# Kernel tuning notes

Hardware: AMD Instinct MI355X
Metric: run time of the kernel (lower is better)

Reference implementation:

```python
import jax, jax.numpy as jnp
import numpy as np

B, T, S, D, K = 512, 49, 200, 512, 128


def setup_inputs() -> dict:
    key = jax.random.key(0)
    ks = jax.random.split(key, 8)
    return {
        "ifeature": jax.random.normal(ks[0], (B, T, D), dtype=jnp.float32),
        "tfeature_h": jax.random.normal(ks[1], (B, S, D), dtype=jnp.float32),
        "w_Dense_Vi_0": jax.random.normal(ks[2], (D, K), dtype=jnp.float32) * 0.05,
        "w_Dense_Vt_0": jax.random.normal(ks[3], (D, K), dtype=jnp.float32) * 0.05,
        "w_Dense_Pi_0": jax.random.normal(ks[4], (2 * K, 1), dtype=jnp.float32) * 0.05,
        "b_Dense_Pi_0": jnp.zeros((T,), dtype=jnp.float32),
        "w_Dense_Vi_1": jax.random.normal(ks[5], (D, K), dtype=jnp.float32) * 0.05,
        "w_Dense_Vt_1": jax.random.normal(ks[6], (D, K), dtype=jnp.float32) * 0.05,
        "w_Dense_Pi_1": jax.random.normal(ks[7], (2 * K, 1), dtype=jnp.float32) * 0.05,
        "b_Dense_Pi_1": jnp.zeros((S,), dtype=jnp.float32),
    }


def reference(ifeature, tfeature_h, w_Dense_Vi_0, w_Dense_Vt_0, w_Dense_Pi_0,
              b_Dense_Pi_0, w_Dense_Vi_1, w_Dense_Vt_1, w_Dense_Pi_1, b_Dense_Pi_1):
    # tfeature: mean-pooled text, [B, D]
    tfeature = jnp.mean(tfeature_h, axis=1)

    # --- attention over image regions (title_len) ---
    w_Vi_0 = jnp.einsum('btd,dk->btk', ifeature, w_Dense_Vi_0)          # [B,T,K]
    w_Vt_0 = (tfeature @ w_Dense_Vt_0)[:, None, :]                      # [B,1,K] broadcast to T
    Hi = jnp.tanh(jnp.concatenate(
        [w_Vi_0, jnp.broadcast_to(w_Vt_0, w_Vi_0.shape)], axis=-1))     # [B,T,2K]
    Hi_w_b = jnp.einsum('btk,k->bt', Hi, w_Dense_Pi_0[:, 0]) + b_Dense_Pi_0
    Pi = jax.nn.softmax(Hi_w_b, axis=-1)                                # [B,T]
    Vi = jnp.einsum('bt,btd->bd', Pi, ifeature)                         # attended image feature

    # --- attention over text tokens (seq_len) ---
    w_Vi_1 = (Vi @ w_Dense_Vi_1)[:, None, :]                            # [B,1,K]
    w_Vt_1 = jnp.einsum('bsd,dk->bsk', tfeature_h, w_Dense_Vt_1)        # [B,S,K]
    Ht = jnp.tanh(jnp.concatenate(
        [jnp.broadcast_to(w_Vi_1, w_Vt_1.shape), w_Vt_1], axis=-1))     # [B,S,2K]
    Ht_b = jnp.einsum('bsk,k->bs', Ht, w_Dense_Pi_1[:, 0]) + b_Dense_Pi_1
    Pt = jax.nn.softmax(Ht_b, axis=-1)                                  # [B,S]

    # NOTE: original call() returns Pt_Vt (weighted tokens), not the pooled Vt.
    Pt_Vt = Pt[:, :, None] * tfeature_h                                 # [B,S,D]
    return Pt_Vt
```

## Files before the change

### kernel.cpp

```cpp
#include <hip/hip_runtime.h>
#include <math.h>

#define BB 512
#define SS 200
#define DD 512
#define KK 128
#define RR (BB * SS)

typedef __attribute__((ext_vector_type(8))) short bf16x8;
typedef __attribute__((ext_vector_type(4))) short bf16x4;
typedef __attribute__((ext_vector_type(4))) float f32x4;

__device__ inline unsigned short f2bf(float f) {
    union { float f; unsigned int u; } v; v.f = f;
    unsigned int r = v.u + 0x7FFFu + ((v.u >> 16) & 1u);
    return (unsigned short)(r >> 16);
}

__device__ inline float fast_tanh(float x) {
    x = fminf(10.f, fmaxf(-10.f, x));
    float t = exp2f(x * 2.885390081777927f);
    return (t - 1.f) * __builtin_amdgcn_rcpf(t + 1.f);
}

__global__ void wt_kernel(const float* __restrict__ W, unsigned short* __restrict__ Wt2) {
    int i = blockIdx.x * 256 + threadIdx.x;
    int j = i & 7;
    int l = (i >> 3) & 63;
    int n = (i >> 9) & 7;
    int t = i >> 12;
    int k = n * 16 + (l & 15);
    int d = t * 32 + (l >> 4) * 8 + j;
    Wt2[i] = f2bf(W[d * KK + k]);
}

__global__ __launch_bounds__(256, 4) void logits_kernel(
    const float* __restrict__ tfh,
    const unsigned short* __restrict__ Wt2,
    const float* __restrict__ wpk,
    const float* __restrict__ bias,
    float* __restrict__ logits)
{
    __shared__ unsigned short As[128][40];

    int tid = threadIdx.x;
    int w   = tid >> 6;
    int l   = tid & 63;
    int l15 = l & 15;
    int g   = l >> 4;
    int brow = blockIdx.x * 128;

    int r0 = tid >> 3;
    int c4 = tid & 7;
    const float* ap = tfh + (size_t)(brow + r0) * DD + c4 * 4;

    const unsigned short* bp = Wt2 + (size_t)l * 8;

    f32x4 acc[2][8];
    #pragma unroll
    for (int m = 0; m < 2; ++m)
        #pragma unroll
        for (int n = 0; n < 8; ++n) acc[m][n] = (f32x4){0.f, 0.f, 0.f, 0.f};

    for (int t = 0; t < 16; ++t) {
        int d0 = t * 32;
        #pragma unroll
        for (int jj = 0; jj < 4; ++jj) {
            float4 v = *(const float4*)(ap + d0 + (size_t)(32 * jj) * DD);
            bf16x4 p;
            p[0] = (short)f2bf(v.x); p[1] = (short)f2bf(v.y);
            p[2] = (short)f2bf(v.z); p[3] = (short)f2bf(v.w);
            *(bf16x4*)&As[r0 + 32 * jj][c4 * 4] = p;
        }
        __syncthreads();
        bf16x8 af0 = *(const bf16x8*)&As[w * 32 + l15][g * 8];
        bf16x8 af1 = *(const bf16x8*)&As[w * 32 + 16 + l15][g * 8];
        const unsigned short* bt = bp + (size_t)t * (8 * 64 * 8);
        #pragma unroll
        for (int nb = 0; nb < 4; ++nb) {
            bf16x8 b0 = *(const bf16x8*)(bt + (2 * nb) * 512);
            bf16x8 b1 = *(const bf16x8*)(bt + (2 * nb + 1) * 512);
            acc[0][2*nb]   = __builtin_amdgcn_mfma_f32_16x16x32_bf16(af0, b0, acc[0][2*nb],   0, 0, 0);
            acc[1][2*nb]   = __builtin_amdgcn_mfma_f32_16x16x32_bf16(af1, b0, acc[1][2*nb],   0, 0, 0);
            acc[0][2*nb+1] = __builtin_amdgcn_mfma_f32_16x16x32_bf16(af0, b1, acc[0][2*nb+1], 0, 0, 0);
            acc[1][2*nb+1] = __builtin_amdgcn_mfma_f32_16x16x32_bf16(af1, b1, acc[1][2*nb+1], 0, 0, 0);
        }
        __syncthreads();
    }

    float wv[8];
    #pragma unroll
    for (int n = 0; n < 8; ++n) wv[n] = wpk[n * 16 + l15];

    float rs[2][4];
    #pragma unroll
    for (int m = 0; m < 2; ++m)
        #pragma unroll
        for (int r = 0; r < 4; ++r) rs[m][r] = 0.f;
    #pragma unroll
    for (int m = 0; m < 2; ++m)
        #pragma unroll
        for (int n = 0; n < 8; ++n)
            #pragma unroll
            for (int r = 0; r < 4; ++r)
                rs[m][r] += fast_tanh(acc[m][n][r]) * wv[n];
    #pragma unroll
    for (int m = 0; m < 2; ++m)
        #pragma unroll
        for (int r = 0; r < 4; ++r) {
            float v = rs[m][r];
            v += __shfl_xor(v, 1, 64);
            v += __shfl_xor(v, 2, 64);
            v += __shfl_xor(v, 4, 64);
            v += __shfl_xor(v, 8, 64);
            rs[m][r] = v;
        }
    if (l15 == 0) {
        #pragma unroll
        for (int m = 0; m < 2; ++m)
            #pragma unroll
            for (int r = 0; r < 4; ++r) {
                int grow = brow + w * 32 + m * 16 + g * 4 + r;
                logits[grow] = rs[m][r] + bias[grow % SS];
            }
    }
}

__global__ __launch_bounds__(1024) void softmax_mul_kernel(
    const float* __restrict__ logits,
    const float* __restrict__ tfh,
    float* __restrict__ out)
{
    int b = blockIdx.x;
    int tid = threadIdx.x;
    __shared__ float Pt[SS];
    __shared__ float wpart[16];

    float v = (tid < SS) ? logits[(size_t)b * SS + tid] : -INFINITY;
    float m = v;
    #pragma unroll
    for (int off = 32; off > 0; off >>= 1) m = fmaxf(m, __shfl_xor(m, off, 64));
    if ((tid & 63) == 0) wpart[tid >> 6] = m;
    __syncthreads();
    m = -INFINITY;
    #pragma unroll
    for (int i = 0; i < 16; ++i) m = fmaxf(m, wpart[i]);
    float e = (tid < SS) ? expf(v - m) : 0.f;
    float ssum = e;
    #pragma unroll
    for (int off = 32; off > 0; off >>= 1) ssum += __shfl_xor(ssum, off, 64);
    __syncthreads();
    if ((tid & 63) == 0) wpart[tid >> 6] = ssum;
    __syncthreads();
    ssum = 0.f;
    #pragma unroll
    for (int i = 0; i < 16; ++i) ssum += wpart[i];
    if (tid < SS) Pt[tid] = e / ssum;
    __syncthreads();

    const f32x4* src = (const f32x4*)(tfh + (size_t)b * SS * DD);
    f32x4*       dst = (f32x4*)(out + (size_t)b * SS * DD);
    const int n4 = SS * DD / 4;
    for (int i = tid; i < n4; i += 1024) {
        float p = Pt[i >> 7];
        f32x4 x = src[i];
        x = x * p;
        __builtin_nontemporal_store(x, dst + i);
    }
}

extern "C" void kernel_launch(void* const* d_in, const int* in_sizes, int n_in,
                              void* d_out, int out_size, void* d_ws, size_t ws_size,
                              hipStream_t stream) {
    const float* tfh   = (const float*)d_in[1];
    const float* wVt1  = (const float*)d_in[7];
    const float* wp1   = (const float*)d_in[8];
    const float* bias1 = (const float*)d_in[9];
    float* out = (float*)d_out;

    unsigned short* Wt2 = (unsigned short*)d_ws;
    float* logits = (float*)((char*)d_ws + 16 * 8 * 64 * 8 * sizeof(unsigned short));

    wt_kernel<<<(16 * 8 * 64 * 8) / 256, 256, 0, stream>>>(wVt1, Wt2);
    logits_kernel<<<RR / 128, 256, 0, stream>>>(tfh, Wt2, wp1 + KK, bias1, logits);
    softmax_mul_kernel<<<BB, 1024, 0, stream>>>(logits, tfh, out);
}
```

Before: 116.5 us.

## Pre-convert activations to bf16 MFMA fragment layout and double-buffer weights in LDS

Adds a separate pass that converts tfeature_h to bf16 and stores it already in MFMA fragment order. A new logits kernel then loads A fragments straight from global memory with register prefetch, and stages the weights in double-buffered LDS so only one barrier is needed per k-step. This removes the in-kernel conversion and LDS round-trip for A. In exchange it costs an extra pass over the 210MB input that writes about 105MB of bf16, and it needs a large workspace, falling back to the old kernel when the workspace is too small.

```diff
diff --git a/kernel.cpp b/kernel.cpp
--- a/kernel.cpp
+++ b/kernel.cpp
@@ -15,6 +15,15 @@
     union { float f; unsigned int u; } v; v.f = f;
     unsigned int r = v.u + 0x7FFFu + ((v.u >> 16) & 1u);
     return (unsigned short)(r >> 16);
+}
+
+__device__ inline bf16x8 pack8(const float4& a, const float4& b) {
+    bf16x8 p;
+    p[0] = (short)f2bf(a.x); p[1] = (short)f2bf(a.y);
+    p[2] = (short)f2bf(a.z); p[3] = (short)f2bf(a.w);
+    p[4] = (short)f2bf(b.x); p[5] = (short)f2bf(b.y);
+    p[6] = (short)f2bf(b.z); p[7] = (short)f2bf(b.w);
+    return p;
 }
 
 __device__ inline float fast_tanh(float x) {
@@ -34,6 +43,120 @@
     Wt2[i] = f2bf(W[d * KK + k]);
 }
 
+__global__ __launch_bounds__(256) void conv_kernel(
+    const float* __restrict__ tfh, unsigned short* __restrict__ bfA)
+{
+    size_t i = (size_t)blockIdx.x * 256 + threadIdx.x;
+    int l   = (int)(i & 63);
+    int sub = (int)((i >> 6) & 7);
+    int t   = (int)((i >> 9) & 15);
+    size_t rt = i >> 13;
+    size_t row = rt * 128 + sub * 16 + (l & 15);
+    int d = t * 32 + (l >> 4) * 8;
+    const float* s = tfh + row * DD + d;
+    float4 v0 = *(const float4*)s;
+    float4 v1 = *(const float4*)(s + 4);
+    *(bf16x8*)(bfA + i * 8) = pack8(v0, v1);
+}
+
+__global__ __launch_bounds__(256, 4) void logits_frag2_kernel(
+    const unsigned short* __restrict__ bfA,
+    const unsigned short* __restrict__ Wt2,
+    const float* __restrict__ wpk,
+    const float* __restrict__ bias,
+    float* __restrict__ logits)
+{
+    __shared__ unsigned short Bs[2][4096];
+
+    int tid = threadIdx.x;
+    int w   = tid >> 6;
+    int l   = tid & 63;
+    int l15 = l & 15;
+    int g   = l >> 4;
+    int rt  = blockIdx.x;
+    int brow = rt * 128;
+
+    const unsigned short* ap = bfA + ((((size_t)rt * 16) * 8 + w * 2) * 64 + l) * 8;
+    const unsigned short* bsrc = Wt2 + tid * 16;
+
+    f32x4 acc[2][8];
+    #pragma unroll
+    for (int m = 0; m < 2; ++m)
+        #pragma unroll
+        for (int n = 0; n < 8; ++n) acc[m][n] = (f32x4){0.f, 0.f, 0.f, 0.f};
+
+    {
+        bf16x8 s0 = *(const bf16x8*)(bsrc);
+        bf16x8 s1 = *(const bf16x8*)(bsrc + 8);
+        *(bf16x8*)&Bs[0][tid * 16]     = s0;
+        *(bf16x8*)&Bs[0][tid * 16 + 8] = s1;
+    }
+    bf16x8 a0 = *(const bf16x8*)(ap);
+    bf16x8 a1 = *(const bf16x8*)(ap + 512);
+    __syncthreads();
+
+    for (int t = 0; t < 16; ++t) {
+        int buf = t & 1;
+        bf16x8 na0, na1, sb0, sb1;
+        if (t < 15) {
+            size_t off = (size_t)(t + 1) * 4096;
+            na0 = *(const bf16x8*)(ap + off);
+            na1 = *(const bf16x8*)(ap + off + 512);
+            sb0 = *(const bf16x8*)(bsrc + off);
+            sb1 = *(const bf16x8*)(bsrc + off + 8);
+        }
+        #pragma unroll
+        for (int n = 0; n < 8; ++n) {
+            bf16x8 bf = *(const bf16x8*)&Bs[buf][n * 512 + l * 8];
+            acc[0][n] = __builtin_amdgcn_mfma_f32_16x16x32_bf16(a0, bf, acc[0][n], 0, 0, 0);
+            acc[1][n] = __builtin_amdgcn_mfma_f32_16x16x32_bf16(a1, bf, acc[1][n], 0, 0, 0);
+        }
+        if (t < 15) {
+            *(bf16x8*)&Bs[buf ^ 1][tid * 16]     = sb0;
+            *(bf16x8*)&Bs[buf ^ 1][tid * 16 + 8] = sb1;
+        }
+        __syncthreads();
+        a0 = na0; a1 = na1;
+    }
+
+    float wv[8];
+    #pragma unroll
+    for (int n = 0; n < 8; ++n) wv[n] = wpk[n * 16 + l15];
+
+    float rs[2][4];
+    #pragma unroll
+    for (int m = 0; m < 2; ++m)
+        #pragma unroll
+        for (int r = 0; r < 4; ++r) rs[m][r] = 0.f;
+    #pragma unroll
+    for (int m = 0; m < 2; ++m)
+        #pragma unroll
+        for (int n = 0; n < 8; ++n)
+            #pragma unroll
+            for (int r = 0; r < 4; ++r)
+                rs[m][r] += fast_tanh(acc[m][n][r]) * wv[n];
+    #pragma unroll
+    for (int m = 0; m < 2; ++m)
+        #pragma unroll
+        for (int r = 0; r < 4; ++r) {
+            float v = rs[m][r];
+            v += __shfl_xor(v, 1, 64);
+            v += __shfl_xor(v, 2, 64);
+            v += __shfl_xor(v, 4, 64);
+            v += __shfl_xor(v, 8, 64);
+            rs[m][r] = v;
+        }
+    if (l15 == 0) {
+        #pragma unroll
+        for (int m = 0; m < 2; ++m)
+            #pragma unroll
+            for (int r = 0; r < 4; ++r) {
+                int grow = brow + w * 32 + m * 16 + g * 4 + r;
+                logits[grow] = rs[m][r] + bias[grow % SS];
+            }
+    }
+}
+
 __global__ __launch_bounds__(256, 4) void logits_kernel(
     const float* __restrict__ tfh,
     const unsigned short* __restrict__ Wt2,
@@ -42,18 +165,15 @@
     float* __restrict__ logits)
 {
     __shared__ unsigned short As[128][40];
-
     int tid = threadIdx.x;
     int w   = tid >> 6;
     int l   = tid & 63;
     int l15 = l & 15;
     int g   = l >> 4;
     int brow = blockIdx.x * 128;
-
     int r0 = tid >> 3;
     int c4 = tid & 7;
     const float* ap = tfh + (size_t)(brow + r0) * DD + c4 * 4;
-
     const unsigned short* bp = Wt2 + (size_t)l * 8;
 
     f32x4 acc[2][8];
@@ -91,7 +211,6 @@
     float wv[8];
     #pragma unroll
     for (int n = 0; n < 8; ++n) wv[n] = wpk[n * 16 + l15];
-
     float rs[2][4];
     #pragma unroll
     for (int m = 0; m < 2; ++m)
@@ -179,9 +298,16 @@
     float* out = (float*)d_out;
 
     unsigned short* Wt2 = (unsigned short*)d_ws;
-    float* logits = (float*)((char*)d_ws + 16 * 8 * 64 * 8 * sizeof(unsigned short));
+    float* logits = (float*)((char*)d_ws + (128 << 10));
+    unsigned short* bfA = (unsigned short*)((char*)d_ws + (1 << 20));
+    const size_t need = (size_t)(1 << 20) + (size_t)RR * DD * 2;
 
     wt_kernel<<<(16 * 8 * 64 * 8) / 256, 256, 0, stream>>>(wVt1, Wt2);
-    logits_kernel<<<RR / 128, 256, 0, stream>>>(tfh, Wt2, wp1 + KK, bias1, logits);
+    if (ws_size >= need) {
+        conv_kernel<<<(int)(((size_t)RR * DD / 8) / 256), 256, 0, stream>>>(tfh, bfA);
+        logits_frag2_kernel<<<RR / 128, 256, 0, stream>>>(bfA, Wt2, wp1 + KK, bias1, logits);
+    } else {
+        logits_kernel<<<RR / 128, 256, 0, stream>>>(tfh, Wt2, wp1 + KK, bias1, logits);
+    }
     softmax_mul_kernel<<<BB, 1024, 0, stream>>>(logits, tfh, out);
 }
```

After: 167.2 us. 1.43x slower.

## Stage weight tiles in shared memory and double the K-step per iteration

Applied to the files above, without the earlier changes.

The weight matrix is now stored as a plain transposed bf16 [K][D] array. Each block stages a 128x64 slice of it into LDS next to the activation tile, where before every wave read pre-swizzled fragments straight from global memory. The K-loop step grows from 32 to 64, which halves the number of barrier pairs, and the occupancy hint drops from 4 to 3 blocks to make room for the larger LDS footprint. The aim is fewer global/L2 weight reads and less synchronisation overhead, at the cost of more LDS use and possibly lower occupancy.

```diff
diff --git a/kernel.cpp b/kernel.cpp
--- a/kernel.cpp
+++ b/kernel.cpp
@@ -23,25 +23,21 @@
     return (t - 1.f) * __builtin_amdgcn_rcpf(t + 1.f);
 }
 
-__global__ void wt_kernel(const float* __restrict__ W, unsigned short* __restrict__ Wt2) {
+__global__ void wt_kernel(const float* __restrict__ W, unsigned short* __restrict__ Wt) {
     int i = blockIdx.x * 256 + threadIdx.x;
-    int j = i & 7;
-    int l = (i >> 3) & 63;
-    int n = (i >> 9) & 7;
-    int t = i >> 12;
-    int k = n * 16 + (l & 15);
-    int d = t * 32 + (l >> 4) * 8 + j;
-    Wt2[i] = f2bf(W[d * KK + k]);
+    int col = i >> 9, d = i & 511;
+    Wt[i] = f2bf(W[d * KK + col]);
 }
 
-__global__ __launch_bounds__(256, 4) void logits_kernel(
+__global__ __launch_bounds__(256, 3) void logits_kernel(
     const float* __restrict__ tfh,
-    const unsigned short* __restrict__ Wt2,
+    const unsigned short* __restrict__ Wt,
     const float* __restrict__ wpk,
     const float* __restrict__ bias,
     float* __restrict__ logits)
 {
-    __shared__ unsigned short As[128][40];
+    __shared__ unsigned short As[128][72];
+    __shared__ unsigned short Bs[128][72];
 
     int tid = threadIdx.x;
     int w   = tid >> 6;
@@ -50,11 +46,13 @@
     int g   = l >> 4;
     int brow = blockIdx.x * 128;
 
-    int r0 = tid >> 3;
-    int c4 = tid & 7;
-    const float* ap = tfh + (size_t)(brow + r0) * DD + c4 * 4;
+    int arow = tid >> 4;
+    int ac4  = tid & 15;
+    const float* ap = tfh + (size_t)(brow + arow) * DD + ac4 * 4;
 
-    const unsigned short* bp = Wt2 + (size_t)l * 8;
+    int bkrow = tid >> 3;
+    int bc8   = tid & 7;
+    const unsigned short* bp = Wt + (size_t)bkrow * DD + bc8 * 8;
 
     f32x4 acc[2][8];
     #pragma unroll
@@ -62,28 +60,32 @@
         #pragma unroll
         for (int n = 0; n < 8; ++n) acc[m][n] = (f32x4){0.f, 0.f, 0.f, 0.f};
 
-    for (int t = 0; t < 16; ++t) {
-        int d0 = t * 32;
+    for (int it = 0; it < 8; ++it) {
+        int d0 = it * 64;
         #pragma unroll
-        for (int jj = 0; jj < 4; ++jj) {
-            float4 v = *(const float4*)(ap + d0 + (size_t)(32 * jj) * DD);
+        for (int j = 0; j < 8; ++j) {
+            float4 v = *(const float4*)(ap + d0 + (size_t)(16 * j) * DD);
             bf16x4 p;
             p[0] = (short)f2bf(v.x); p[1] = (short)f2bf(v.y);
             p[2] = (short)f2bf(v.z); p[3] = (short)f2bf(v.w);
-            *(bf16x4*)&As[r0 + 32 * jj][c4 * 4] = p;
+            *(bf16x4*)&As[arow + 16 * j][ac4 * 4] = p;
+        }
+        #pragma unroll
+        for (int j = 0; j < 4; ++j) {
+            bf16x8 q = *(const bf16x8*)(bp + d0 + (size_t)(32 * j) * DD);
+            *(bf16x8*)&Bs[bkrow + 32 * j][bc8 * 8] = q;
         }
         __syncthreads();
-        bf16x8 af0 = *(const bf16x8*)&As[w * 32 + l15][g * 8];
-        bf16x8 af1 = *(const bf16x8*)&As[w * 32 + 16 + l15][g * 8];
-        const unsigned short* bt = bp + (size_t)t * (8 * 64 * 8);
         #pragma unroll
-        for (int nb = 0; nb < 4; ++nb) {
-            bf16x8 b0 = *(const bf16x8*)(bt + (2 * nb) * 512);
-            bf16x8 b1 = *(const bf16x8*)(bt + (2 * nb + 1) * 512);
-            acc[0][2*nb]   = __builtin_amdgcn_mfma_f32_16x16x32_bf16(af0, b0, acc[0][2*nb],   0, 0, 0);
-            acc[1][2*nb]   = __builtin_amdgcn_mfma_f32_16x16x32_bf16(af1, b0, acc[1][2*nb],   0, 0, 0);
-            acc[0][2*nb+1] = __builtin_amdgcn_mfma_f32_16x16x32_bf16(af0, b1, acc[0][2*nb+1], 0, 0, 0);
-            acc[1][2*nb+1] = __builtin_amdgcn_mfma_f32_16x16x32_bf16(af1, b1, acc[1][2*nb+1], 0, 0, 0);
+        for (int h = 0; h < 2; ++h) {
+            bf16x8 af0 = *(const bf16x8*)&As[w * 32 + l15][h * 32 + g * 8];
+            bf16x8 af1 = *(const bf16x8*)&As[w * 32 + 16 + l15][h * 32 + g * 8];
+            #pragma unroll
+            for (int n = 0; n < 8; ++n) {
+                bf16x8 bf = *(const bf16x8*)&Bs[n * 16 + l15][h * 32 + g * 8];
+                acc[0][n] = __builtin_amdgcn_mfma_f32_16x16x32_bf16(af0, bf, acc[0][n], 0, 0, 0);
+                acc[1][n] = __builtin_amdgcn_mfma_f32_16x16x32_bf16(af1, bf, acc[1][n], 0, 0, 0);
+            }
         }
         __syncthreads();
     }
@@ -178,10 +180,10 @@
     const float* bias1 = (const float*)d_in[9];
     float* out = (float*)d_out;
 
-    unsigned short* Wt2 = (unsigned short*)d_ws;
-    float* logits = (float*)((char*)d_ws + 16 * 8 * 64 * 8 * sizeof(unsigned short));
+    unsigned short* Wt = (unsigned short*)d_ws;
+    float* logits = (float*)((char*)d_ws + (128 << 10));
 
-    wt_kernel<<<(16 * 8 * 64 * 8) / 256, 256, 0, stream>>>(wVt1, Wt2);
-    logits_kernel<<<RR / 128, 256, 0, stream>>>(tfh, Wt2, wp1 + KK, bias1, logits);
+    wt_kernel<<<KK * DD / 256, 256, 0, stream>>>(wVt1, Wt);
+    logits_kernel<<<RR / 128, 256, 0, stream>>>(tfh, Wt, wp1 + KK, bias1, logits);
     softmax_mul_kernel<<<BB, 1024, 0, stream>>>(logits, tfh, out);
 }
```

New measurement: 123.8 us. 1.06x slower.

## Load A rows directly into registers per wave, drop LDS staging and syncs

Applied to the files above, without the earlier changes.

The logits GEMM now has each wave own 16 rows. It loads the full 512-wide A fragment from global straight into 16 bf16x8 registers, with no shared-memory staging or __syncthreads. Blocks cover 64 rows instead of 128, launch bounds change to 3 waves per EU, and the logits workspace offset is moved. This removes LDS traffic and barriers but halves the reuse of each B fragment per wave. It also raises register pressure and uses an uncoalesced row-strided global load pattern.

```diff
diff --git a/kernel.cpp b/kernel.cpp
--- a/kernel.cpp
+++ b/kernel.cpp
@@ -8,13 +8,21 @@
 #define RR (BB * SS)
 
 typedef __attribute__((ext_vector_type(8))) short bf16x8;
-typedef __attribute__((ext_vector_type(4))) short bf16x4;
 typedef __attribute__((ext_vector_type(4))) float f32x4;
 
 __device__ inline unsigned short f2bf(float f) {
     union { float f; unsigned int u; } v; v.f = f;
     unsigned int r = v.u + 0x7FFFu + ((v.u >> 16) & 1u);
     return (unsigned short)(r >> 16);
+}
+
+__device__ inline bf16x8 pack8(const float4& a, const float4& b) {
+    bf16x8 p;
+    p[0] = (short)f2bf(a.x); p[1] = (short)f2bf(a.y);
+    p[2] = (short)f2bf(a.z); p[3] = (short)f2bf(a.w);
+    p[4] = (short)f2bf(b.x); p[5] = (short)f2bf(b.y);
+    p[6] = (short)f2bf(b.z); p[7] = (short)f2bf(b.w);
+    return p;
 }
 
 __device__ inline float fast_tanh(float x) {
@@ -34,95 +42,73 @@
     Wt2[i] = f2bf(W[d * KK + k]);
 }
 
-__global__ __launch_bounds__(256, 4) void logits_kernel(
+__global__ __launch_bounds__(256, 3) void logits_kernel(
     const float* __restrict__ tfh,
     const unsigned short* __restrict__ Wt2,
     const float* __restrict__ wpk,
     const float* __restrict__ bias,
     float* __restrict__ logits)
 {
-    __shared__ unsigned short As[128][40];
-
     int tid = threadIdx.x;
     int w   = tid >> 6;
     int l   = tid & 63;
     int l15 = l & 15;
     int g   = l >> 4;
-    int brow = blockIdx.x * 128;
+    int W   = blockIdx.x * 4 + w;
+    int row = W * 16 + l15;
 
-    int r0 = tid >> 3;
-    int c4 = tid & 7;
-    const float* ap = tfh + (size_t)(brow + r0) * DD + c4 * 4;
-
+    const float* a = tfh + (size_t)row * DD + g * 8;
     const unsigned short* bp = Wt2 + (size_t)l * 8;
 
-    f32x4 acc[2][8];
+    bf16x8 abf[16];
     #pragma unroll
-    for (int m = 0; m < 2; ++m)
-        #pragma unroll
-        for (int n = 0; n < 8; ++n) acc[m][n] = (f32x4){0.f, 0.f, 0.f, 0.f};
+    for (int t = 0; t < 16; ++t) {
+        float4 v0 = *(const float4*)(a + t * 32);
+        float4 v1 = *(const float4*)(a + t * 32 + 4);
+        abf[t] = pack8(v0, v1);
+    }
 
+    f32x4 acc[8];
+    #pragma unroll
+    for (int n = 0; n < 8; ++n) acc[n] = (f32x4){0.f, 0.f, 0.f, 0.f};
+
+    #pragma unroll
     for (int t = 0; t < 16; ++t) {
-        int d0 = t * 32;
-        #pragma unroll
-        for (int jj = 0; jj < 4; ++jj) {
-            float4 v = *(const float4*)(ap + d0 + (size_t)(32 * jj) * DD);
-            bf16x4 p;
-            p[0] = (short)f2bf(v.x); p[1] = (short)f2bf(v.y);
-            p[2] = (short)f2bf(v.z); p[3] = (short)f2bf(v.w);
-            *(bf16x4*)&As[r0 + 32 * jj][c4 * 4] = p;
-        }
-        __syncthreads();
-        bf16x8 af0 = *(const bf16x8*)&As[w * 32 + l15][g * 8];
-        bf16x8 af1 = *(const bf16x8*)&As[w * 32 + 16 + l15][g * 8];
         const unsigned short* bt = bp + (size_t)t * (8 * 64 * 8);
         #pragma unroll
-        for (int nb = 0; nb < 4; ++nb) {
-            bf16x8 b0 = *(const bf16x8*)(bt + (2 * nb) * 512);
-            bf16x8 b1 = *(const bf16x8*)(bt + (2 * nb + 1) * 512);
-            acc[0][2*nb]   = __builtin_amdgcn_mfma_f32_16x16x32_bf16(af0, b0, acc[0][2*nb],   0, 0, 0);
-            acc[1][2*nb]   = __builtin_amdgcn_mfma_f32_16x16x32_bf16(af1, b0, acc[1][2*nb],   0, 0, 0);
-            acc[0][2*nb+1] = __builtin_amdgcn_mfma_f32_16x16x32_bf16(af0, b1, acc[0][2*nb+1], 0, 0, 0);
-            acc[1][2*nb+1] = __builtin_amdgcn_mfma_f32_16x16x32_bf16(af1, b1, acc[1][2*nb+1], 0, 0, 0);
+        for (int n = 0; n < 8; ++n) {
+            bf16x8 bf = *(const bf16x8*)(bt + n * 512);
+            acc[n] = __builtin_amdgcn_mfma_f32_16x16x32_bf16(abf[t], bf, acc[n], 0, 0, 0);
         }
-        __syncthreads();
     }
 
     float wv[8];
     #pragma unroll
     for (int n = 0; n < 8; ++n) wv[n] = wpk[n * 16 + l15];
 
-    float rs[2][4];
+    float rs[4];
     #pragma unroll
-    for (int m = 0; m < 2; ++m)
+    for (int r = 0; r < 4; ++r) rs[r] = 0.f;
+    #pragma unroll
+    for (int n = 0; n < 8; ++n)
         #pragma unroll
-        for (int r = 0; r < 4; ++r) rs[m][r] = 0.f;
+        for (int r = 0; r < 4; ++r)
+            rs[r] += fast_tanh(acc[n][r]) * wv[n];
     #pragma unroll
-    for (int m = 0; m < 2; ++m)
-        #pragma unroll
-        for (int n = 0; n < 8; ++n)
-            #pragma unroll
-            for (int r = 0; r < 4; ++r)
-                rs[m][r] += fast_tanh(acc[m][n][r]) * wv[n];
-    #pragma unroll
-    for (int m = 0; m < 2; ++m)
+    for (int r = 0; r < 4; ++r) {
+        float v = rs[r];
+        v += __shfl_xor(v, 1, 64);
+        v += __shfl_xor(v, 2, 64);
+        v += __shfl_xor(v, 4, 64);
+        v += __shfl_xor(v, 8, 64);
+        rs[r] = v;
+    }
+    if (l15 == 0) {
         #pragma unroll
         for (int r = 0; r < 4; ++r) {
-            float v = rs[m][r];
-            v += __shfl_xor(v, 1, 64);
-            v += __shfl_xor(v, 2, 64);
-            v += __shfl_xor(v, 4, 64);
-            v += __shfl_xor(v, 8, 64);
-            rs[m][r] = v;
+            int grow = W * 16 + g * 4 + r;
+            logits[grow] = rs[r] + bias[grow % SS];
         }
-    if (l15 == 0) {
-        #pragma unroll
-        for (int m = 0; m < 2; ++m)
-            #pragma unroll
-            for (int r = 0; r < 4; ++r) {
-                int grow = brow + w * 32 + m * 16 + g * 4 + r;
-                logits[grow] = rs[m][r] + bias[grow % SS];
-            }
     }
 }
 
@@ -179,9 +165,9 @@
     float* out = (float*)d_out;
 
     unsigned short* Wt2 = (unsigned short*)d_ws;
-    float* logits = (float*)((char*)d_ws + 16 * 8 * 64 * 8 * sizeof(unsigned short));
+    float* logits = (float*)((char*)d_ws + (128 << 10));
 
     wt_kernel<<<(16 * 8 * 64 * 8) / 256, 256, 0, stream>>>(wVt1, Wt2);
-    logits_kernel<<<RR / 128, 256, 0, stream>>>(tfh, Wt2, wp1 + KK, bias1, logits);
+    logits_kernel<<<RR / 64, 256, 0, stream>>>(tfh, Wt2, wp1 + KK, bias1, logits);
     softmax_mul_kernel<<<BB, 1024, 0, stream>>>(logits, tfh, out);
 }
```

Result: slower. 131.2 us (+12.6%).
